# Kernel optimization log

Measured on AMD Instinct MI355X. Metric: run time of the kernel, lower is better.

## Reference

```python
import jax, jax.numpy as jnp
import numpy as np

D_K = 128


def setup_inputs() -> dict:
    key = jax.random.key(0)
    ks = jax.random.split(key, 10)
    B, S, D, TP, TE, DK = 4, 4096, 1024, 16, 64, D_K
    sc = lambda fan_in: 1.0 / np.sqrt(fan_in)
    return {
        "x": jax.random.normal(ks[0], (B, S, D), jnp.float32),
        "time_points": jax.random.normal(ks[1], (B, TP, TE), jnp.float32),
        "Wq": jax.random.normal(ks[2], (D, DK), jnp.float32) * sc(D),
        "bq": jnp.zeros((DK,), jnp.float32),
        "Wk": jax.random.normal(ks[3], (D, DK), jnp.float32) * sc(D),
        "bk": jnp.zeros((DK,), jnp.float32),
        "Wv": jax.random.normal(ks[4], (D, DK), jnp.float32) * sc(D),
        "bv": jnp.zeros((DK,), jnp.float32),
        "Wt": jax.random.normal(ks[5], (TE, DK), jnp.float32) * sc(TE),
        "bt": jnp.zeros((DK,), jnp.float32),
    }


def reference(x, time_points, Wq, bq, Wk, bk, Wv, bv, Wt, bt):
    B, S, _ = x.shape
    Q = x @ Wq + bq              # [B,S,dk]
    K = x @ Wk + bk              # [B,S,dk]
    V = x @ Wv + bv              # [B,S,dk]
    E = time_points @ Wt + bt    # [B,TP,dk] = time_emb
    # T = repeat(E, S times along dim 1). Then T^T @ T = S * E^T E and
    # ||T||_F = sqrt(S) * ||E||_F, so we never materialize T.
    S_f = jnp.asarray(S, jnp.float32)
    EtE = jnp.einsum('btd,bte->bde', E, E)            # [B,dk,dk]
    T_norm = jnp.sqrt(S_f * jnp.sum(E * E, axis=(1, 2), keepdims=False))  # [B]
    T_scaled = (S_f * EtE) / (T_norm[:, None, None] + 1e-8)  # [B,dk,dk]
    QT = jnp.einsum('bsd,bde->bse', Q, T_scaled)      # [B,S,dk]
    scores = jnp.einsum('bse,bte->bst', QT, K)        # [B,S,S]
    scores = scores / jnp.sqrt(jnp.asarray(D_K, jnp.float32))
    attn = jax.nn.softmax(scores, axis=-1)            # [B,S,S]
    out = jnp.einsum('bst,btd->bsd', attn, V)         # [B,S,dk]
    return out, attn
```

## Files before the change

### kernel.cpp

```cpp
#include <hip/hip_runtime.h>
#include <math.h>

#define BB 4
#define SS 4096
#define DD 1024
#define TPp 16
#define TEe 64
#define DKk 128

typedef __attribute__((ext_vector_type(8))) short short8;
typedef __attribute__((ext_vector_type(4))) float floatx4;
typedef __attribute__((ext_vector_type(16))) float floatx16;

#define BSTRIDE 524288
#define WFRAG 131072

static __device__ inline short f2bf(float f) {
  union { float f; unsigned u; } v; v.f = f;
  unsigned r = v.u + 0x7fff + ((v.u >> 16) & 1);
  return (short)(r >> 16);
}
static __device__ inline float bf2f(short s) {
  union { unsigned u; float f; } v; v.u = ((unsigned)(unsigned short)s) << 16;
  return v.f;
}

__global__ __launch_bounds__(256) void temb_kernel(const float* __restrict__ tp,
                                                   const float* __restrict__ Wt,
                                                   const float* __restrict__ bt,
                                                   const float* __restrict__ bq,
                                                   float* __restrict__ Tws,
                                                   float* __restrict__ bqtws) {
  __shared__ float sE[TPp * DKk];
  __shared__ float sB[TPp];
  __shared__ float red[256];
  const int p = blockIdx.x, b = blockIdx.y;
  const int tid = threadIdx.x;
  float lsq = 0.f;
  for (int l = 0; l < 8; ++l) {
    int idx = tid + 256 * l;
    int i = idx >> 7, j = idx & 127;
    float a = bt[j];
    for (int c = 0; c < TEe; ++c)
      a += tp[((size_t)b * TPp + i) * TEe + c] * Wt[c * DKk + j];
    sE[idx] = a;
    lsq += a * a;
  }
  red[tid] = lsq;
  __syncthreads();
  for (int s2 = 128; s2 > 0; s2 >>= 1) {
    if (tid < s2) red[tid] += red[tid + s2];
    __syncthreads();
  }
  const float total = red[0];
  const float scale = (float)SS / (sqrtf((float)SS * total) + 1e-8f);
  if (tid < TPp) {
    float a = 0.f;
    for (int d2 = 0; d2 < DKk; ++d2) a += bq[d2] * sE[tid * DKk + d2];
    sB[tid] = a;
  }
  __syncthreads();
  for (int l = 0; l < 8; ++l) {
    int idx = p * 2048 + tid + 256 * l;
    int d2 = idx >> 7, e = idx & 127;
    float a = 0.f;
    #pragma unroll
    for (int t = 0; t < TPp; ++t) a += sE[t * DKk + d2] * sE[t * DKk + e];
    Tws[(size_t)b * DKk * DKk + idx] = scale * a;
  }
  if (p == 0 && tid < DKk) {
    float a = 0.f;
    #pragma unroll
    for (int t = 0; t < TPp; ++t) a += sB[t] * sE[t * DKk + tid];
    bqtws[b * DKk + tid] = scale * a;
  }
}

__global__ __launch_bounds__(128) void wqp_kernel(const float* __restrict__ Wq,
                                                  const float* __restrict__ Tws,
                                                  short* __restrict__ WqphF,
                                                  short* __restrict__ WqplF) {
  __shared__ float sW[DKk];
  const int m = blockIdx.x, b = blockIdx.y;
  const int e = threadIdx.x;
  sW[e] = Wq[(size_t)m * DKk + e];
  __syncthreads();
  const float* Tb = Tws + (size_t)b * DKk * DKk;
  float a = 0.f;
  #pragma unroll 8
  for (int d2 = 0; d2 < DKk; ++d2) a += sW[d2] * Tb[d2 * DKk + e];
  const size_t off = (size_t)b * WFRAG +
      (size_t)((e >> 5) * 64 + (m >> 4)) * 512 + (32 * ((m >> 3) & 1) + (e & 31)) * 8 +
      (m & 7);
  short hh = f2bf(a);
  WqphF[off] = hh;
  WqplF[off] = f2bf(a - bf2f(hh));
}

__global__ __launch_bounds__(256) void wcast_kernel(const float* __restrict__ Wk,
                                                    const float* __restrict__ Wv,
                                                    short* __restrict__ WkhF,
                                                    short* __restrict__ WklF,
                                                    short* __restrict__ WvhF,
                                                    short* __restrict__ WvlF) {
  const float* W = blockIdx.y ? Wv : Wk;
  short* H = blockIdx.y ? WvhF : WkhF;
  short* L = blockIdx.y ? WvlF : WklF;
  const int ks = blockIdx.x;
  const int wave = threadIdx.x >> 6, lane = threadIdx.x & 63;
  const int n = wave * 32 + (lane & 31);
  const int k0 = ks * 16 + (lane >> 5) * 8;
  short8 h, l;
  #pragma unroll
  for (int j = 0; j < 8; ++j) {
    float v = W[(size_t)(k0 + j) * DKk + n];
    short hh = f2bf(v);
    h[j] = hh;
    l[j] = f2bf(v - bf2f(hh));
  }
  const size_t off = ((size_t)wave * 64 + ks) * 512 + lane * 8;
  *(short8*)&H[off] = h;
  *(short8*)&L[off] = l;
}

__global__ __launch_bounds__(256, 2) void proj_kernel(const float* __restrict__ x,
                                                      const short* __restrict__ WqphF,
                                                      const short* __restrict__ WqplF,
                                                      const short* __restrict__ WkhF,
                                                      const short* __restrict__ WklF,
                                                      const short* __restrict__ WvhF,
                                                      const short* __restrict__ WvlF,
                                                      const float* __restrict__ bqt,
                                                      const float* __restrict__ bk,
                                                      const float* __restrict__ bv,
                                                      short* __restrict__ QTh,
                                                      short* __restrict__ QTl,
                                                      short* __restrict__ Kh,
                                                      short* __restrict__ Kl,
                                                      short* __restrict__ VT) {
  __shared__ float xs[32 * 66];
  const int tileG = blockIdx.x;
  const int b = tileG >> 7, tileL = tileG & 127;
  const int rowbase = tileG * 32;
  const int tid = threadIdx.x, wave = tid >> 6, lane = tid & 63;
  const int l31 = lane & 31, half = lane >> 5;
  const short* B0h = WqphF + (size_t)b * WFRAG + (size_t)wave * 32768;
  const short* B0l = WqplF + (size_t)b * WFRAG + (size_t)wave * 32768;
  const short* B1h = WkhF + (size_t)wave * 32768;
  const short* B1l = WklF + (size_t)wave * 32768;
  const short* B2h = WvhF + (size_t)wave * 32768;
  const short* B2l = WvlF + (size_t)wave * 32768;
  floatx16 acc0, acc1, acc2;
  #pragma unroll
  for (int r = 0; r < 16; ++r) { acc0[r] = 0.f; acc1[r] = 0.f; acc2[r] = 0.f; }
  const int sr = tid >> 3, sc = (tid & 7) * 8;
  const float* xrow = &x[(size_t)(rowbase + sr) * DD + sc];
  float4 p0 = *(const float4*)xrow;
  float4 p1 = *(const float4*)(xrow + 4);
  for (int kc = 0; kc < 16; ++kc) {
    __syncthreads();
    float* dst = &xs[sr * 66 + sc];
    dst[0] = p0.x; dst[1] = p0.y; dst[2] = p0.z; dst[3] = p0.w;
    dst[4] = p1.x; dst[5] = p1.y; dst[6] = p1.z; dst[7] = p1.w;
    if (kc < 15) {
      p0 = *(const float4*)(xrow + (kc + 1) * 64);
      p1 = *(const float4*)(xrow + (kc + 1) * 64 + 4);
    }
    __syncthreads();
    #pragma unroll
    for (int ks = 0; ks < 4; ++ks) {
      const float* ap = &xs[l31 * 66 + ks * 16 + half * 8];
      short8 aH, aL;
      #pragma unroll
      for (int j = 0; j < 8; ++j) {
        float v = ap[j];
        short hh = f2bf(v);
        aH[j] = hh;
        aL[j] = f2bf(v - bf2f(hh));
      }
      const size_t boff = (size_t)(kc * 4 + ks) * 512 + lane * 8;
      short8 bh, bl;
      bh = *(const short8*)(B0h + boff); bl = *(const short8*)(B0l + boff);
      acc0 = __builtin_amdgcn_mfma_f32_32x32x16_bf16(aL, bh, acc0, 0, 0, 0);
      acc0 = __builtin_amdgcn_mfma_f32_32x32x16_bf16(aH, bl, acc0, 0, 0, 0);
      acc0 = __builtin_amdgcn_mfma_f32_32x32x16_bf16(aH, bh, acc0, 0, 0, 0);
      bh = *(const short8*)(B1h + boff); bl = *(const short8*)(B1l + boff);
      acc1 = __builtin_amdgcn_mfma_f32_32x32x16_bf16(aL, bh, acc1, 0, 0, 0);
      acc1 = __builtin_amdgcn_mfma_f32_32x32x16_bf16(aH, bl, acc1, 0, 0, 0);
      acc1 = __builtin_amdgcn_mfma_f32_32x32x16_bf16(aH, bh, acc1, 0, 0, 0);
      bh = *(const short8*)(B2h + boff); bl = *(const short8*)(B2l + boff);
      acc2 = __builtin_amdgcn_mfma_f32_32x32x16_bf16(aL, bh, acc2, 0, 0, 0);
      acc2 = __builtin_amdgcn_mfma_f32_32x32x16_bf16(aH, bl, acc2, 0, 0, 0);
      acc2 = __builtin_amdgcn_mfma_f32_32x32x16_bf16(aH, bh, acc2, 0, 0, 0);
    }
  }
  const int f = wave * 32 + l31;
  const int fks = f >> 4, fh = (f >> 3) & 1, fj = f & 7;
  const size_t qkbase =
      (size_t)b * BSTRIDE + (size_t)tileL * 4096 + (size_t)fks * 512 + fj;
  const float biasq = bqt[b * DKk + f];
  const float biask = bk[f];
  #pragma unroll
  for (int reg = 0; reg < 16; ++reg) {
    const int t = (reg & 3) + 8 * (reg >> 2) + 4 * half;
    const size_t off = qkbase + (size_t)(fh * 32 + t) * 8;
    float v = acc0[reg] + biasq;
    short hh = f2bf(v);
    QTh[off] = hh;
    QTl[off] = f2bf(v - bf2f(hh));
    v = acc1[reg] + biask;
    hh = f2bf(v);
    Kh[off] = hh;
    Kl[off] = f2bf(v - bf2f(hh));
  }
  const float biasv = bv[f];
  #pragma unroll
  for (int g = 0; g < 4; ++g) {
    short4 s4;
    s4.x = f2bf(acc2[4 * g + 0] + biasv);
    s4.y = f2bf(acc2[4 * g + 1] + biasv);
    s4.z = f2bf(acc2[4 * g + 2] + biasv);
    s4.w = f2bf(acc2[4 * g + 3] + biasv);
    const size_t off = (size_t)b * BSTRIDE +
        (size_t)(wave * 256 + tileL * 2 + (g >> 1)) * 512 +
        (size_t)((g & 1) * 32 + l31) * 8 + 4 * half;
    *(short4*)&VT[off] = s4;
  }
}

__global__ __launch_bounds__(256, 2) void ml_kernel(const short* __restrict__ QTh,
                                                    const short* __restrict__ QTl,
                                                    const short* __restrict__ Kh,
                                                    const short* __restrict__ Kl,
                                                    float* __restrict__ mrow,
                                                    float* __restrict__ linv) {
  __shared__ float smM[4][32], smL[4][32];
  const int id = blockIdx.x;
  const int xcd = id & 7;
  const int b = xcd >> 1;
  const int tile = ((id >> 3) << 1) + (xcd & 1);
  const int rowbase = tile * 32;
  const int tid = threadIdx.x;
  const int wave = tid >> 6, lane = tid & 63;
  const int l31 = lane & 31;
  const float sc = 0.088388347648318447f;
  const size_t qbase = (size_t)b * BSTRIDE + (size_t)tile * 4096 + lane * 8;
  short8 qh[8], ql[8];
  #pragma unroll
  for (int ks = 0; ks < 8; ++ks) {
    qh[ks] = *(const short8*)(QTh + qbase + ks * 512);
    ql[ks] = *(const short8*)(QTl + qbase + ks * 512);
  }
  float m = -INFINITY, l = 0.f;
  for (int ct = wave; ct < 128; ct += 4) {
    const size_t kbase = (size_t)b * BSTRIDE + (size_t)ct * 4096 + lane * 8;
    floatx16 acc;
    #pragma unroll
    for (int r = 0; r < 16; ++r) acc[r] = 0.f;
    #pragma unroll
    for (int ks = 0; ks < 8; ++ks) {
      short8 kh = *(const short8*)(Kh + kbase + ks * 512);
      short8 kl = *(const short8*)(Kl + kbase + ks * 512);
      acc = __builtin_amdgcn_mfma_f32_32x32x16_bf16(kh, qh[ks], acc, 0, 0, 0);
      acc = __builtin_amdgcn_mfma_f32_32x32x16_bf16(kh, ql[ks], acc, 0, 0, 0);
      acc = __builtin_amdgcn_mfma_f32_32x32x16_bf16(kl, qh[ks], acc, 0, 0, 0);
    }
    float s[16];
    float tmax = -INFINITY;
    #pragma unroll
    for (int r = 0; r < 16; ++r) { s[r] = acc[r] * sc; tmax = fmaxf(tmax, s[r]); }
    const float mn = fmaxf(m, tmax);
    float ps = 0.f;
    #pragma unroll
    for (int r = 0; r < 16; ++r) ps += __expf(s[r] - mn);
    l = l * __expf(m - mn) + ps;
    m = mn;
  }
  {
    const float mo = __shfl_xor(m, 32, 64);
    const float lo = __shfl_xor(l, 32, 64);
    const float mn = fmaxf(m, mo);
    l = l * __expf(m - mn) + lo * __expf(mo - mn);
    m = mn;
  }
  if (lane < 32) { smM[wave][l31] = m; smL[wave][l31] = l; }
  __syncthreads();
  if (tid < 32) {
    float mm = smM[0][tid], ll = smL[0][tid];
    #pragma unroll
    for (int w = 1; w < 4; ++w) {
      const float mo = smM[w][tid], lo = smL[w][tid];
      const float mn = fmaxf(mm, mo);
      ll = ll * __expf(mm - mn) + lo * __expf(mo - mn);
      mm = mn;
    }
    mrow[b * SS + rowbase + tid] = mm;
    linv[b * SS + rowbase + tid] = 1.0f / ll;
  }
}

__global__ __launch_bounds__(256, 2) void pv_kernel(const short* __restrict__ QTh,
                                                    const short* __restrict__ QTl,
                                                    const short* __restrict__ Kh,
                                                    const short* __restrict__ Kl,
                                                    const short* __restrict__ VT,
                                                    float* __restrict__ attn,
                                                    const float* __restrict__ mrow,
                                                    const float* __restrict__ linv,
                                                    float* __restrict__ outp) {
  __shared__ float sAcc[3][4][64][16];
  const int id = blockIdx.x;
  const int xcd = id & 7;
  const int b = xcd >> 1;
  const int tile = ((id >> 3) << 1) + (xcd & 1);
  const int rowbase = tile * 32;
  const int tid = threadIdx.x;
  const int wave = tid >> 6, lane = tid & 63;
  const int l31 = lane & 31, half = lane >> 5;
  const float sc = 0.088388347648318447f;
  const size_t qbase = (size_t)b * BSTRIDE + (size_t)tile * 4096 + lane * 8;
  short8 qh[8], ql[8];
  #pragma unroll
  for (int ks = 0; ks < 8; ++ks) {
    qh[ks] = *(const short8*)(QTh + qbase + ks * 512);
    ql[ks] = *(const short8*)(QTl + qbase + ks * 512);
  }
  const float m_i = mrow[b * SS + rowbase + l31];
  const float li = linv[b * SS + rowbase + l31];
  float* arow = attn + (size_t)b * SS * SS + (size_t)(rowbase + l31) * SS + 4 * half;
  const short* vtb = VT + (size_t)b * BSTRIDE + lane * 8;
  floatx16 pacc[4];
  #pragma unroll
  for (int dt = 0; dt < 4; ++dt)
    #pragma unroll
    for (int r = 0; r < 16; ++r) pacc[dt][r] = 0.f;
  for (int ct = wave; ct < 128; ct += 4) {
    const size_t kbase = (size_t)b * BSTRIDE + (size_t)ct * 4096 + lane * 8;
    floatx16 acc;
    #pragma unroll
    for (int r = 0; r < 16; ++r) acc[r] = 0.f;
    #pragma unroll
    for (int ks = 0; ks < 8; ++ks) {
      short8 kh = *(const short8*)(Kh + kbase + ks * 512);
      short8 kl = *(const short8*)(Kl + kbase + ks * 512);
      acc = __builtin_amdgcn_mfma_f32_32x32x16_bf16(kh, qh[ks], acc, 0, 0, 0);
      acc = __builtin_amdgcn_mfma_f32_32x32x16_bf16(kh, ql[ks], acc, 0, 0, 0);
      acc = __builtin_amdgcn_mfma_f32_32x32x16_bf16(kl, qh[ks], acc, 0, 0, 0);
    }
    float p[16];
    #pragma unroll
    for (int r = 0; r < 16; ++r) p[r] = __expf(acc[r] * sc - m_i) * li;
    #pragma unroll
    for (int g = 0; g < 4; ++g) {
      floatx4 o = {p[4 * g], p[4 * g + 1], p[4 * g + 2], p[4 * g + 3]};
      __builtin_nontemporal_store(o, (floatx4*)(arow + ct * 32 + 8 * g));
    }
    short8 af0, af1;
    #pragma unroll
    for (int rr = 0; rr < 4; ++rr) {
      const float shl = __shfl_xor(p[rr], 32, 64);
      const float shh = __shfl_xor(p[rr + 4], 32, 64);
      af0[rr] = f2bf(half ? shh : p[rr]);
      af0[rr + 4] = f2bf(half ? p[rr + 4] : shl);
      const float shl2 = __shfl_xor(p[rr + 8], 32, 64);
      const float shh2 = __shfl_xor(p[rr + 12], 32, 64);
      af1[rr] = f2bf(half ? shh2 : p[rr + 8]);
      af1[rr + 4] = f2bf(half ? p[rr + 12] : shl2);
    }
    #pragma unroll
    for (int dt = 0; dt < 4; ++dt) {
      short8 v0 = *(const short8*)(vtb + (size_t)(dt * 256 + ct * 2) * 512);
      pacc[dt] = __builtin_amdgcn_mfma_f32_32x32x16_bf16(af0, v0, pacc[dt], 0, 0, 0);
      short8 v1 = *(const short8*)(vtb + (size_t)(dt * 256 + ct * 2 + 1) * 512);
      pacc[dt] = __builtin_amdgcn_mfma_f32_32x32x16_bf16(af1, v1, pacc[dt], 0, 0, 0);
    }
  }
  if (wave > 0) {
    #pragma unroll
    for (int dt = 0; dt < 4; ++dt)
      #pragma unroll
      for (int r = 0; r < 16; ++r) sAcc[wave - 1][dt][lane][r] = pacc[dt][r];
  }
  __syncthreads();
  if (wave == 0) {
    #pragma unroll
    for (int dt = 0; dt < 4; ++dt)
      #pragma unroll
      for (int r = 0; r < 16; ++r) {
        const int q = (r & 3) + 8 * (r >> 2) + 4 * half;
        const float v = pacc[dt][r] + sAcc[0][dt][lane][r] + sAcc[1][dt][lane][r] +
                        sAcc[2][dt][lane][r];
        outp[((size_t)b * SS + rowbase + q) * DKk + dt * 32 + l31] = v;
      }
  }
}

extern "C" void kernel_launch(void* const* d_in, const int* in_sizes, int n_in,
                              void* d_out, int out_size, void* d_ws, size_t ws_size,
                              hipStream_t stream) {
  const float* x  = (const float*)d_in[0];
  const float* tp = (const float*)d_in[1];
  const float* Wq = (const float*)d_in[2];
  const float* bq = (const float*)d_in[3];
  const float* Wk = (const float*)d_in[4];
  const float* bk = (const float*)d_in[5];
  const float* Wv = (const float*)d_in[6];
  const float* bv = (const float*)d_in[7];
  const float* Wt = (const float*)d_in[8];
  const float* bt = (const float*)d_in[9];
  float* out  = (float*)d_out;
  float* attn = out + (size_t)BB * SS * DKk;
  float* ws = (float*)d_ws;
  float* Tws   = ws;
  float* bqt   = ws + 65536;
  short* WqphF = (short*)(ws + 66048);
  short* WqplF = (short*)(ws + 328192);
  short* WkhF  = (short*)(ws + 590336);
  short* WklF  = (short*)(ws + 655872);
  short* WvhF  = (short*)(ws + 721408);
  short* WvlF  = (short*)(ws + 786944);
  short* QTh   = (short*)(ws + 852480);
  short* QTl   = (short*)(ws + 1901056);
  short* Kh    = (short*)(ws + 2949632);
  short* Kl    = (short*)(ws + 3998208);
  short* VT    = (short*)(ws + 5046784);
  float* mrow  = ws + 6095360;
  float* lin   = ws + 6111744;

  temb_kernel<<<dim3(8, 4), 256, 0, stream>>>(tp, Wt, bt, bq, Tws, bqt);
  wqp_kernel<<<dim3(1024, 4), 128, 0, stream>>>(Wq, Tws, WqphF, WqplF);
  wcast_kernel<<<dim3(64, 2), 256, 0, stream>>>(Wk, Wv, WkhF, WklF, WvhF, WvlF);
  proj_kernel<<<512, 256, 0, stream>>>(x, WqphF, WqplF, WkhF, WklF, WvhF, WvlF,
                                       bqt, bk, bv, QTh, QTl, Kh, Kl, VT);
  ml_kernel<<<512, 256, 0, stream>>>(QTh, QTl, Kh, Kl, mrow, lin);
  pv_kernel<<<512, 256, 0, stream>>>(QTh, QTl, Kh, Kl, VT, attn, mrow, lin, out);
}
```

Before: 709.4 us.

## Pre-split x into bf16 fragments and split projection grid by Q/K/V

Adds an xcast kernel that converts x once into hi/lo bf16 MFMA fragment layout. The projection kernel then runs three times as many blocks, one per Q, K or V region, with no shared memory or barriers and higher occupancy. The projection, ml and pv kernels also split their MFMA chains into two independent accumulators to hide MFMA latency. The cost is an extra kernel launch, a larger workspace, and re-reading the A fragments once per region.

```diff
diff --git a/kernel.cpp b/kernel.cpp
--- a/kernel.cpp
+++ b/kernel.cpp
@@ -14,6 +14,7 @@
 
 #define BSTRIDE 524288
 #define WFRAG 131072
+#define XTILE 32768
 
 static __device__ inline short f2bf(float f) {
   union { float f; unsigned u; } v; v.f = f;
@@ -123,7 +124,35 @@
   *(short8*)&L[off] = l;
 }
 
-__global__ __launch_bounds__(256, 2) void proj_kernel(const float* __restrict__ x,
+__global__ __launch_bounds__(256) void xcast_kernel(const float* __restrict__ x,
+                                                    short* __restrict__ XAh,
+                                                    short* __restrict__ XAl) {
+  const int tileG = blockIdx.x;
+  const int rowbase = tileG * 32;
+  const int tid = threadIdx.x;
+  const int t = tid & 31, khalf = (tid >> 5) & 1, w = tid >> 6;
+  const size_t abase = (size_t)tileG * XTILE + (size_t)(tid & 63) * 8;
+  const float* xr = x + (size_t)(rowbase + t) * DD + khalf * 8;
+  #pragma unroll
+  for (int it = 0; it < 16; ++it) {
+    const int ks = it * 4 + w;
+    float4 u0 = *(const float4*)(xr + ks * 16);
+    float4 u1 = *(const float4*)(xr + ks * 16 + 4);
+    const float v[8] = {u0.x, u0.y, u0.z, u0.w, u1.x, u1.y, u1.z, u1.w};
+    short8 h, l;
+    #pragma unroll
+    for (int j = 0; j < 8; ++j) {
+      short hh = f2bf(v[j]);
+      h[j] = hh;
+      l[j] = f2bf(v[j] - bf2f(hh));
+    }
+    *(short8*)&XAh[abase + (size_t)ks * 512] = h;
+    *(short8*)&XAl[abase + (size_t)ks * 512] = l;
+  }
+}
+
+__global__ __launch_bounds__(256, 4) void proj_kernel(const short* __restrict__ XAh,
+                                                      const short* __restrict__ XAl,
                                                       const short* __restrict__ WqphF,
                                                       const short* __restrict__ WqplF,
                                                       const short* __restrict__ WkhF,
@@ -138,93 +167,73 @@
                                                       short* __restrict__ Kh,
                                                       short* __restrict__ Kl,
                                                       short* __restrict__ VT) {
-  __shared__ float xs[32 * 66];
-  const int tileG = blockIdx.x;
+  const int id = blockIdx.x;
+  const int region = id >> 9, tileG = id & 511;
   const int b = tileG >> 7, tileL = tileG & 127;
-  const int rowbase = tileG * 32;
   const int tid = threadIdx.x, wave = tid >> 6, lane = tid & 63;
   const int l31 = lane & 31, half = lane >> 5;
-  const short* B0h = WqphF + (size_t)b * WFRAG + (size_t)wave * 32768;
-  const short* B0l = WqplF + (size_t)b * WFRAG + (size_t)wave * 32768;
-  const short* B1h = WkhF + (size_t)wave * 32768;
-  const short* B1l = WklF + (size_t)wave * 32768;
-  const short* B2h = WvhF + (size_t)wave * 32768;
-  const short* B2l = WvlF + (size_t)wave * 32768;
-  floatx16 acc0, acc1, acc2;
-  #pragma unroll
-  for (int r = 0; r < 16; ++r) { acc0[r] = 0.f; acc1[r] = 0.f; acc2[r] = 0.f; }
-  const int sr = tid >> 3, sc = (tid & 7) * 8;
-  const float* xrow = &x[(size_t)(rowbase + sr) * DD + sc];
-  float4 p0 = *(const float4*)xrow;
-  float4 p1 = *(const float4*)(xrow + 4);
-  for (int kc = 0; kc < 16; ++kc) {
-    __syncthreads();
-    float* dst = &xs[sr * 66 + sc];
-    dst[0] = p0.x; dst[1] = p0.y; dst[2] = p0.z; dst[3] = p0.w;
-    dst[4] = p1.x; dst[5] = p1.y; dst[6] = p1.z; dst[7] = p1.w;
-    if (kc < 15) {
-      p0 = *(const float4*)(xrow + (kc + 1) * 64);
-      p1 = *(const float4*)(xrow + (kc + 1) * 64 + 4);
-    }
-    __syncthreads();
-    #pragma unroll
-    for (int ks = 0; ks < 4; ++ks) {
-      const float* ap = &xs[l31 * 66 + ks * 16 + half * 8];
-      short8 aH, aL;
-      #pragma unroll
-      for (int j = 0; j < 8; ++j) {
-        float v = ap[j];
-        short hh = f2bf(v);
-        aH[j] = hh;
-        aL[j] = f2bf(v - bf2f(hh));
-      }
-      const size_t boff = (size_t)(kc * 4 + ks) * 512 + lane * 8;
-      short8 bh, bl;
-      bh = *(const short8*)(B0h + boff); bl = *(const short8*)(B0l + boff);
-      acc0 = __builtin_amdgcn_mfma_f32_32x32x16_bf16(aL, bh, acc0, 0, 0, 0);
-      acc0 = __builtin_amdgcn_mfma_f32_32x32x16_bf16(aH, bl, acc0, 0, 0, 0);
-      acc0 = __builtin_amdgcn_mfma_f32_32x32x16_bf16(aH, bh, acc0, 0, 0, 0);
-      bh = *(const short8*)(B1h + boff); bl = *(const short8*)(B1l + boff);
-      acc1 = __builtin_amdgcn_mfma_f32_32x32x16_bf16(aL, bh, acc1, 0, 0, 0);
-      acc1 = __builtin_amdgcn_mfma_f32_32x32x16_bf16(aH, bl, acc1, 0, 0, 0);
-      acc1 = __builtin_amdgcn_mfma_f32_32x32x16_bf16(aH, bh, acc1, 0, 0, 0);
-      bh = *(const short8*)(B2h + boff); bl = *(const short8*)(B2l + boff);
-      acc2 = __builtin_amdgcn_mfma_f32_32x32x16_bf16(aL, bh, acc2, 0, 0, 0);
-      acc2 = __builtin_amdgcn_mfma_f32_32x32x16_bf16(aH, bl, acc2, 0, 0, 0);
-      acc2 = __builtin_amdgcn_mfma_f32_32x32x16_bf16(aH, bh, acc2, 0, 0, 0);
-    }
-  }
+  const short* BH;
+  const short* BL;
+  if (region == 0)      { BH = WqphF + (size_t)b * WFRAG; BL = WqplF + (size_t)b * WFRAG; }
+  else if (region == 1) { BH = WkhF; BL = WklF; }
+  else                  { BH = WvhF; BL = WvlF; }
+  BH += (size_t)wave * 32768 + (size_t)lane * 8;
+  BL += (size_t)wave * 32768 + (size_t)lane * 8;
+  const short* AH = XAh + (size_t)tileG * XTILE + (size_t)lane * 8;
+  const short* AL = XAl + (size_t)tileG * XTILE + (size_t)lane * 8;
+  floatx16 accE, accO;
+  #pragma unroll
+  for (int r = 0; r < 16; ++r) { accE[r] = 0.f; accO[r] = 0.f; }
+  for (int ks = 0; ks < 64; ks += 2) {
+    short8 a0h = *(const short8*)(AH + (size_t)ks * 512);
+    short8 a0l = *(const short8*)(AL + (size_t)ks * 512);
+    short8 b0h = *(const short8*)(BH + (size_t)ks * 512);
+    short8 b0l = *(const short8*)(BL + (size_t)ks * 512);
+    short8 a1h = *(const short8*)(AH + (size_t)(ks + 1) * 512);
+    short8 a1l = *(const short8*)(AL + (size_t)(ks + 1) * 512);
+    short8 b1h = *(const short8*)(BH + (size_t)(ks + 1) * 512);
+    short8 b1l = *(const short8*)(BL + (size_t)(ks + 1) * 512);
+    accE = __builtin_amdgcn_mfma_f32_32x32x16_bf16(a0l, b0h, accE, 0, 0, 0);
+    accO = __builtin_amdgcn_mfma_f32_32x32x16_bf16(a1l, b1h, accO, 0, 0, 0);
+    accE = __builtin_amdgcn_mfma_f32_32x32x16_bf16(a0h, b0l, accE, 0, 0, 0);
+    accO = __builtin_amdgcn_mfma_f32_32x32x16_bf16(a1h, b1l, accO, 0, 0, 0);
+    accE = __builtin_amdgcn_mfma_f32_32x32x16_bf16(a0h, b0h, accE, 0, 0, 0);
+    accO = __builtin_amdgcn_mfma_f32_32x32x16_bf16(a1h, b1h, accO, 0, 0, 0);
+  }
+  floatx16 acc;
+  #pragma unroll
+  for (int r = 0; r < 16; ++r) acc[r] = accE[r] + accO[r];
   const int f = wave * 32 + l31;
-  const int fks = f >> 4, fh = (f >> 3) & 1, fj = f & 7;
-  const size_t qkbase =
-      (size_t)b * BSTRIDE + (size_t)tileL * 4096 + (size_t)fks * 512 + fj;
-  const float biasq = bqt[b * DKk + f];
-  const float biask = bk[f];
-  #pragma unroll
-  for (int reg = 0; reg < 16; ++reg) {
-    const int t = (reg & 3) + 8 * (reg >> 2) + 4 * half;
-    const size_t off = qkbase + (size_t)(fh * 32 + t) * 8;
-    float v = acc0[reg] + biasq;
-    short hh = f2bf(v);
-    QTh[off] = hh;
-    QTl[off] = f2bf(v - bf2f(hh));
-    v = acc1[reg] + biask;
-    hh = f2bf(v);
-    Kh[off] = hh;
-    Kl[off] = f2bf(v - bf2f(hh));
-  }
-  const float biasv = bv[f];
-  #pragma unroll
-  for (int g = 0; g < 4; ++g) {
-    short4 s4;
-    s4.x = f2bf(acc2[4 * g + 0] + biasv);
-    s4.y = f2bf(acc2[4 * g + 1] + biasv);
-    s4.z = f2bf(acc2[4 * g + 2] + biasv);
-    s4.w = f2bf(acc2[4 * g + 3] + biasv);
-    const size_t off = (size_t)b * BSTRIDE +
-        (size_t)(wave * 256 + tileL * 2 + (g >> 1)) * 512 +
-        (size_t)((g & 1) * 32 + l31) * 8 + 4 * half;
-    *(short4*)&VT[off] = s4;
+  if (region <= 1) {
+    short* Hp = (region == 0) ? QTh : Kh;
+    short* Lp = (region == 0) ? QTl : Kl;
+    const float bias = (region == 0) ? bqt[b * DKk + f] : bk[f];
+    const int fks = f >> 4, fh = (f >> 3) & 1, fj = f & 7;
+    const size_t qkbase =
+        (size_t)b * BSTRIDE + (size_t)tileL * 4096 + (size_t)fks * 512 + fj;
+    #pragma unroll
+    for (int reg = 0; reg < 16; ++reg) {
+      const int t = (reg & 3) + 8 * (reg >> 2) + 4 * half;
+      const size_t off = qkbase + (size_t)(fh * 32 + t) * 8;
+      float v = acc[reg] + bias;
+      short hh = f2bf(v);
+      Hp[off] = hh;
+      Lp[off] = f2bf(v - bf2f(hh));
+    }
+  } else {
+    const float biasv = bv[f];
+    #pragma unroll
+    for (int g = 0; g < 4; ++g) {
+      short4 s4;
+      s4.x = f2bf(acc[4 * g + 0] + biasv);
+      s4.y = f2bf(acc[4 * g + 1] + biasv);
+      s4.z = f2bf(acc[4 * g + 2] + biasv);
+      s4.w = f2bf(acc[4 * g + 3] + biasv);
+      const size_t off = (size_t)b * BSTRIDE +
+          (size_t)(wave * 256 + tileL * 2 + (g >> 1)) * 512 +
+          (size_t)((g & 1) * 32 + l31) * 8 + 4 * half;
+      *(short4*)&VT[off] = s4;
+    }
   }
 }
 
@@ -254,21 +263,29 @@
   float m = -INFINITY, l = 0.f;
   for (int ct = wave; ct < 128; ct += 4) {
     const size_t kbase = (size_t)b * BSTRIDE + (size_t)ct * 4096 + lane * 8;
-    floatx16 acc;
-    #pragma unroll
-    for (int r = 0; r < 16; ++r) acc[r] = 0.f;
-    #pragma unroll
-    for (int ks = 0; ks < 8; ++ks) {
-      short8 kh = *(const short8*)(Kh + kbase + ks * 512);
-      short8 kl = *(const short8*)(Kl + kbase + ks * 512);
-      acc = __builtin_amdgcn_mfma_f32_32x32x16_bf16(kh, qh[ks], acc, 0, 0, 0);
-      acc = __builtin_amdgcn_mfma_f32_32x32x16_bf16(kh, ql[ks], acc, 0, 0, 0);
-      acc = __builtin_amdgcn_mfma_f32_32x32x16_bf16(kl, qh[ks], acc, 0, 0, 0);
+    floatx16 accA, accB;
+    #pragma unroll
+    for (int r = 0; r < 16; ++r) { accA[r] = 0.f; accB[r] = 0.f; }
+    #pragma unroll
+    for (int ks = 0; ks < 4; ++ks) {
+      short8 kh0 = *(const short8*)(Kh + kbase + ks * 512);
+      short8 kl0 = *(const short8*)(Kl + kbase + ks * 512);
+      short8 kh1 = *(const short8*)(Kh + kbase + (ks + 4) * 512);
+      short8 kl1 = *(const short8*)(Kl + kbase + (ks + 4) * 512);
+      accA = __builtin_amdgcn_mfma_f32_32x32x16_bf16(kh0, qh[ks], accA, 0, 0, 0);
+      accB = __builtin_amdgcn_mfma_f32_32x32x16_bf16(kh1, qh[ks + 4], accB, 0, 0, 0);
+      accA = __builtin_amdgcn_mfma_f32_32x32x16_bf16(kh0, ql[ks], accA, 0, 0, 0);
+      accB = __builtin_amdgcn_mfma_f32_32x32x16_bf16(kh1, ql[ks + 4], accB, 0, 0, 0);
+      accA = __builtin_amdgcn_mfma_f32_32x32x16_bf16(kl0, qh[ks], accA, 0, 0, 0);
+      accB = __builtin_amdgcn_mfma_f32_32x32x16_bf16(kl1, qh[ks + 4], accB, 0, 0, 0);
     }
     float s[16];
     float tmax = -INFINITY;
     #pragma unroll
-    for (int r = 0; r < 16; ++r) { s[r] = acc[r] * sc; tmax = fmaxf(tmax, s[r]); }
+    for (int r = 0; r < 16; ++r) {
+      s[r] = (accA[r] + accB[r]) * sc;
+      tmax = fmaxf(tmax, s[r]);
+    }
     const float mn = fmaxf(m, tmax);
     float ps = 0.f;
     #pragma unroll
@@ -336,20 +353,26 @@
     for (int r = 0; r < 16; ++r) pacc[dt][r] = 0.f;
   for (int ct = wave; ct < 128; ct += 4) {
     const size_t kbase = (size_t)b * BSTRIDE + (size_t)ct * 4096 + lane * 8;
-    floatx16 acc;
-    #pragma unroll
-    for (int r = 0; r < 16; ++r) acc[r] = 0.f;
-    #pragma unroll
-    for (int ks = 0; ks < 8; ++ks) {
-      short8 kh = *(const short8*)(Kh + kbase + ks * 512);
-      short8 kl = *(const short8*)(Kl + kbase + ks * 512);
-      acc = __builtin_amdgcn_mfma_f32_32x32x16_bf16(kh, qh[ks], acc, 0, 0, 0);
-      acc = __builtin_amdgcn_mfma_f32_32x32x16_bf16(kh, ql[ks], acc, 0, 0, 0);
-      acc = __builtin_amdgcn_mfma_f32_32x32x16_bf16(kl, qh[ks], acc, 0, 0, 0);
+    floatx16 accA, accB;
+    #pragma unroll
+    for (int r = 0; r < 16; ++r) { accA[r] = 0.f; accB[r] = 0.f; }
+    #pragma unroll
+    for (int ks = 0; ks < 4; ++ks) {
+      short8 kh0 = *(const short8*)(Kh + kbase + ks * 512);
+      short8 kl0 = *(const short8*)(Kl + kbase + ks * 512);
+      short8 kh1 = *(const short8*)(Kh + kbase + (ks + 4) * 512);
+      short8 kl1 = *(const short8*)(Kl + kbase + (ks + 4) * 512);
+      accA = __builtin_amdgcn_mfma_f32_32x32x16_bf16(kh0, qh[ks], accA, 0, 0, 0);
+      accB = __builtin_amdgcn_mfma_f32_32x32x16_bf16(kh1, qh[ks + 4], accB, 0, 0, 0);
+      accA = __builtin_amdgcn_mfma_f32_32x32x16_bf16(kh0, ql[ks], accA, 0, 0, 0);
+      accB = __builtin_amdgcn_mfma_f32_32x32x16_bf16(kh1, ql[ks + 4], accB, 0, 0, 0);
+      accA = __builtin_amdgcn_mfma_f32_32x32x16_bf16(kl0, qh[ks], accA, 0, 0, 0);
+      accB = __builtin_amdgcn_mfma_f32_32x32x16_bf16(kl1, qh[ks + 4], accB, 0, 0, 0);
     }
     float p[16];
     #pragma unroll
-    for (int r = 0; r < 16; ++r) p[r] = __expf(acc[r] * sc - m_i) * li;
+    for (int r = 0; r < 16; ++r)
+      p[r] = __expf((accA[r] + accB[r]) * sc - m_i) * li;
     #pragma unroll
     for (int g = 0; g < 4; ++g) {
       floatx4 o = {p[4 * g], p[4 * g + 1], p[4 * g + 2], p[4 * g + 3]};
@@ -419,19 +442,23 @@
   short* WklF  = (short*)(ws + 655872);
   short* WvhF  = (short*)(ws + 721408);
   short* WvlF  = (short*)(ws + 786944);
-  short* QTh   = (short*)(ws + 852480);
-  short* QTl   = (short*)(ws + 1901056);
-  short* Kh    = (short*)(ws + 2949632);
-  short* Kl    = (short*)(ws + 3998208);
-  short* VT    = (short*)(ws + 5046784);
-  float* mrow  = ws + 6095360;
-  float* lin   = ws + 6111744;
+  short* XAh   = (short*)(ws + 852480);
+  short* XAl   = (short*)(ws + 9241088);
+  short* QTh   = (short*)(ws + 17629696);
+  short* QTl   = (short*)(ws + 18678272);
+  short* Kh    = (short*)(ws + 19726848);
+  short* Kl    = (short*)(ws + 20775424);
+  short* VT    = (short*)(ws + 21824000);
+  float* mrow  = ws + 22872576;
+  float* lin   = ws + 22888960;
 
   temb_kernel<<<dim3(8, 4), 256, 0, stream>>>(tp, Wt, bt, bq, Tws, bqt);
   wqp_kernel<<<dim3(1024, 4), 128, 0, stream>>>(Wq, Tws, WqphF, WqplF);
   wcast_kernel<<<dim3(64, 2), 256, 0, stream>>>(Wk, Wv, WkhF, WklF, WvhF, WvlF);
-  proj_kernel<<<512, 256, 0, stream>>>(x, WqphF, WqplF, WkhF, WklF, WvhF, WvlF,
-                                       bqt, bk, bv, QTh, QTl, Kh, Kl, VT);
+  xcast_kernel<<<512, 256, 0, stream>>>(x, XAh, XAl);
+  proj_kernel<<<1536, 256, 0, stream>>>(XAh, XAl, WqphF, WqplF, WkhF, WklF,
+                                        WvhF, WvlF, bqt, bk, bv,
+                                        QTh, QTl, Kh, Kl, VT);
   ml_kernel<<<512, 256, 0, stream>>>(QTh, QTl, Kh, Kl, mrow, lin);
   pv_kernel<<<512, 256, 0, stream>>>(QTh, QTl, Kh, Kl, VT, attn, mrow, lin, out);
 }
```

Result: faster. 620.0 us (-12.6%).
